# Kernel optimization log

Measured on AMD Instinct MI355X. Metric: run time of the kernel, lower is better.

The kernel has to match this reference:

```python
import jax, jax.numpy as jnp
import numpy as np

IN_CH, OUT_CH = 32, 32
MODES1, MODES2 = 16, 16
B, L, H, W = 8, 16, 64, 33


def setup_inputs() -> dict:
    key = jax.random.key(0)
    k = jax.random.split(key, 6)
    scale = 1.0 / (IN_CH * OUT_CH)
    wshape = (IN_CH, OUT_CH, MODES1, MODES2)
    return {
        "x_re": jax.random.normal(k[0], (B, L, IN_CH, H, W), dtype=jnp.float32),
        "x_im": jax.random.normal(k[1], (B, L, IN_CH, H, W), dtype=jnp.float32),
        "w1_re": scale * jax.random.normal(k[2], wshape, dtype=jnp.float32),
        "w1_im": scale * jax.random.normal(k[3], wshape, dtype=jnp.float32),
        "w2_re": scale * jax.random.normal(k[4], wshape, dtype=jnp.float32),
        "w2_im": scale * jax.random.normal(k[5], wshape, dtype=jnp.float32),
    }


def _mul2d(x, w):
    # x: [B, L, C_in, m1, m2] complex; w: [C_in, C_out, m1, m2] complex
    return jnp.einsum("blcij,coij->bloij", x, w)


def reference(x_re, x_im, w1_re, w1_im, w2_re, w2_im):
    x = jax.lax.complex(x_re, x_im)          # [B, L, C, H, W] complex64
    w1 = jax.lax.complex(w1_re, w1_im)       # [C_in, C_out, m1, m2]
    w2 = jax.lax.complex(w2_re, w2_im)
    Bx, Lx, Cx, Hx, Wx = x.shape
    m1 = min(Hx, MODES1)
    m2 = min(Wx, MODES2)

    out = jnp.zeros((Bx, Lx, OUT_CH, Hx, Wx), dtype=x.dtype)
    # low positive frequencies (top-left corner)
    out = out.at[:, :, :, :m1, :m2].set(
        _mul2d(x[:, :, :, :m1, :m2], w1[:, :, :m1, :m2]))
    # low negative frequencies along H (bottom-left corner)
    if Hx > 1 and (Hx > MODES1 or Wx > MODES2):
        out = out.at[:, :, :, -m1:, :m2].set(
            _mul2d(x[:, :, :, -m1:, :m2], w2[:, :, :m1, :m2]))
    # return complex result as trailing real/imag dim (float32)
    return jnp.stack([out.real, out.imag], axis=-1)
```

## Files before the change

### kernel.cpp

```cpp
#include <hip/hip_runtime.h>

#define IN_CH 32
#define OUT_CH 32
#define M1 16
#define M2 16
#define H_ 64
#define W_ 33
#define HW (H_*W_)
#define BLPB 4
#define WSTRIDE (OUT_CH*M1*M2)
#define CBATCH 8

__global__ __launch_bounds__(256) void spectral_fused(
    const float* __restrict__ x_re, const float* __restrict__ x_im,
    const float* __restrict__ w1_re, const float* __restrict__ w1_im,
    const float* __restrict__ w2_re, const float* __restrict__ w2_im,
    float* __restrict__ out)
{
    const int tid = threadIdx.x;

    if (blockIdx.x & 1) {
        const int fid = blockIdx.x >> 1;
        const int gtid = fid * 256 + tid;
        const int nthreads = 1024 * 256;

        float4* out4 = (float4*)out;
        const float4 z4 = make_float4(0.f, 0.f, 0.f, 0.f);
        const int totalA = 4096 * 528;
        for (int idx = gtid; idx < totalA; idx += nthreads) {
            int plane = idx / 528;
            int k = idx - plane * 528;
            out4[(long)plane * 1056 + 264 + k] = z4;
        }
        float2* out2 = (float2*)out;
        const float2 z2 = make_float2(0.f, 0.f);
        const int totalB = 4096 * 544;
        for (int idx = gtid; idx < totalB; idx += nthreads) {
            int plane = idx / 544;
            int r = idx - plane * 544;
            int hh = r / 17;
            int t = r - hh * 17;
            int h = hh < 16 ? hh : hh + 32;
            out2[(long)plane * 2112 + h * 33 + 16 + t] = z2;
        }
        return;
    }

    const int cid = blockIdx.x >> 1;
    const int ri = cid >> 5;
    const int chunk = cid & 31;
    const int region = ri >> 4;
    const int i = ri & 15;
    const int h = region ? (48 + i) : i;
    const int bl0 = chunk * BLPB;

    __shared__ float2 xs[BLPB][IN_CH][M2];

    for (int item = tid; item < BLPB * IN_CH * M2; item += 256) {
        int j = item & 15;
        int c = (item >> 4) & 31;
        int b = item >> 9;
        long src = (long)((bl0 + b) * IN_CH + c) * HW + (long)h * W_ + j;
        xs[b][c][j] = make_float2(x_re[src], x_im[src]);
    }
    __syncthreads();

    const int j  = tid & 15;
    const int o0 = tid >> 4;
    const float* __restrict__ wre = (region ? w2_re : w1_re) + (o0 * M1 + i) * M2 + j;
    const float* __restrict__ wim = (region ? w2_im : w1_im) + (o0 * M1 + i) * M2 + j;

    float2 acc0[BLPB], acc1[BLPB];
    #pragma unroll
    for (int b = 0; b < BLPB; ++b) {
        acc0[b] = make_float2(0.f, 0.f);
        acc1[b] = make_float2(0.f, 0.f);
    }

    #pragma unroll 1
    for (int cb = 0; cb < IN_CH; cb += CBATCH) {
        float wr0[CBATCH], wi0[CBATCH], wr1[CBATCH], wi1[CBATCH];
        #pragma unroll
        for (int u = 0; u < CBATCH; ++u) {
            int idx = (cb + u) * WSTRIDE;
            wr0[u] = wre[idx];        wi0[u] = wim[idx];
            wr1[u] = wre[idx + 4096]; wi1[u] = wim[idx + 4096];
        }
        #pragma unroll
        for (int u = 0; u < CBATCH; ++u) {
            #pragma unroll
            for (int b = 0; b < BLPB; ++b) {
                float2 xc = xs[b][cb + u][j];
                acc0[b].x = fmaf(xc.x, wr0[u], acc0[b].x); acc0[b].x = fmaf(-xc.y, wi0[u], acc0[b].x);
                acc0[b].y = fmaf(xc.x, wi0[u], acc0[b].y); acc0[b].y = fmaf( xc.y, wr0[u], acc0[b].y);
                acc1[b].x = fmaf(xc.x, wr1[u], acc1[b].x); acc1[b].x = fmaf(-xc.y, wi1[u], acc1[b].x);
                acc1[b].y = fmaf(xc.x, wi1[u], acc1[b].y); acc1[b].y = fmaf( xc.y, wr1[u], acc1[b].y);
            }
        }
    }

    float2* out2 = (float2*)out;
    #pragma unroll
    for (int b = 0; b < BLPB; ++b) {
        long plane = (long)(bl0 + b) * OUT_CH;
        long d0 = (plane + o0)      * HW + (long)h * W_ + j;
        long d1 = (plane + o0 + 16) * HW + (long)h * W_ + j;
        out2[d0] = acc0[b];
        out2[d1] = acc1[b];
    }
}

extern "C" void kernel_launch(void* const* d_in, const int* in_sizes, int n_in,
                              void* d_out, int out_size, void* d_ws, size_t ws_size,
                              hipStream_t stream) {
    const float* x_re  = (const float*)d_in[0];
    const float* x_im  = (const float*)d_in[1];
    const float* w1_re = (const float*)d_in[2];
    const float* w1_im = (const float*)d_in[3];
    const float* w2_re = (const float*)d_in[4];
    const float* w2_im = (const float*)d_in[5];
    float* out = (float*)d_out;

    spectral_fused<<<dim3(2048), dim3(256), 0, stream>>>(
        x_re, x_im, w1_re, w1_im, w2_re, w2_im, out);
}
```

Baseline: 37.14 us.

## Use bf16x3-split MFMA for the complex mode contraction with a prep kernel

Replaces the scalar FMA complex contraction with two kernels. The first gathers the mode slices of x and the weights, splits each fp32 value into hi and lo bf16 parts, and stores them in a workspace in MFMA fragment layout. The second runs 16x16x32 bf16 MFMAs, using three products per real term to approximate fp32 accuracy, and writes the combined real and imaginary outputs. The zero-fill of the output is split between the two kernels. In exchange it adds a second launch and a round trip through the workspace, and the bf16 split may lose a little precision compared with fp32.

```diff
diff --git a/kernel.cpp b/kernel.cpp
--- a/kernel.cpp
+++ b/kernel.cpp
@@ -1,112 +1,200 @@
 #include <hip/hip_runtime.h>
 
-#define IN_CH 32
-#define OUT_CH 32
-#define M1 16
-#define M2 16
-#define H_ 64
-#define W_ 33
-#define HW (H_*W_)
-#define BLPB 4
-#define WSTRIDE (OUT_CH*M1*M2)
-#define CBATCH 8
-
-__global__ __launch_bounds__(256) void spectral_fused(
+#define HW 2112L
+typedef float f32x4 __attribute__((ext_vector_type(4)));
+typedef short s16x8 __attribute__((ext_vector_type(8)));
+
+#define XT_PLANE 4194304L
+#define WT_PLANE 1048576L
+#define OFF_XHR 0L
+#define OFF_XLR (XT_PLANE)
+#define OFF_XHI (2*XT_PLANE)
+#define OFF_XLI (3*XT_PLANE)
+#define OFF_WHR (4*XT_PLANE)
+#define OFF_WLR (4*XT_PLANE + WT_PLANE)
+#define OFF_WHI (4*XT_PLANE + 2*WT_PLANE)
+#define OFF_WLI (4*XT_PLANE + 3*WT_PLANE)
+
+__device__ __forceinline__ ushort f2bf(float f) {
+    unsigned u = __float_as_uint(f);
+    u += 0x7FFF + ((u >> 16) & 1);
+    return (ushort)(u >> 16);
+}
+__device__ __forceinline__ void split_bf(float v, ushort& hi, ushort& lo) {
+    hi = f2bf(v);
+    float hf = __uint_as_float(((unsigned)hi) << 16);
+    lo = f2bf(v - hf);
+}
+
+__global__ __launch_bounds__(256) void spectral_prep(
     const float* __restrict__ x_re, const float* __restrict__ x_im,
     const float* __restrict__ w1_re, const float* __restrict__ w1_im,
     const float* __restrict__ w2_re, const float* __restrict__ w2_im,
-    float* __restrict__ out)
+    float* __restrict__ out, char* __restrict__ ws)
 {
     const int tid = threadIdx.x;
-
-    if (blockIdx.x & 1) {
-        const int fid = blockIdx.x >> 1;
-        const int gtid = fid * 256 + tid;
-        const int nthreads = 1024 * 256;
-
+    const int bid = blockIdx.x;
+    __shared__ float lds[32][16][17];
+
+    if (bid < 256) {
+        const int r = bid >> 7, i = (bid >> 3) & 15, mt = bid & 7;
+        const int h = r ? 48 + i : i;
+        const int j = tid >> 4, row = tid & 15;
+        const int modeLin = (r * 16 + i) * 16 + j;
+        #pragma unroll 1
+        for (int pass = 0; pass < 2; ++pass) {
+            const float* src = pass ? x_im : x_re;
+            if (pass) __syncthreads();
+            for (int it = 0; it < 32; ++it) {
+                int idx = it * 256 + tid;
+                int jj = idx & 15, rr = idx >> 4;
+                int c = rr >> 4, rw = rr & 15;
+                int bl = mt * 16 + rw;
+                lds[c][rw][jj] = src[(long)(bl * 32 + c) * HW + h * 33 + jj];
+            }
+            __syncthreads();
+            s16x8* ph = (s16x8*)(ws + (pass ? OFF_XHI : OFF_XHR));
+            s16x8* pl = (s16x8*)(ws + (pass ? OFF_XLI : OFF_XLR));
+            #pragma unroll
+            for (int kg = 0; kg < 4; ++kg) {
+                s16x8 vh, vl;
+                #pragma unroll
+                for (int e = 0; e < 8; ++e) {
+                    ushort a, b;
+                    split_bf(lds[kg * 8 + e][row][j], a, b);
+                    vh[e] = (short)a; vl[e] = (short)b;
+                }
+                long off = (long)(modeLin * 8 + mt) * 64 + kg * 16 + row;
+                ph[off] = vh;
+                pl[off] = vl;
+            }
+        }
+    } else if (bid < 320) {
+        const int widx = bid - 256;
+        const int r = widx >> 5, i = (widx >> 1) & 15, nt = widx & 1;
+        const float* wre = r ? w2_re : w1_re;
+        const float* wim = r ? w2_im : w1_im;
+        const int j = tid >> 4, col = tid & 15, o = nt * 16 + col;
+        const int modeLin = (r * 16 + i) * 16 + j;
+        s16x8* phr = (s16x8*)(ws + OFF_WHR);
+        s16x8* plr = (s16x8*)(ws + OFF_WLR);
+        s16x8* phi = (s16x8*)(ws + OFF_WHI);
+        s16x8* pli = (s16x8*)(ws + OFF_WLI);
+        #pragma unroll
+        for (int kg = 0; kg < 4; ++kg) {
+            s16x8 hr, lr, hi2, li2;
+            #pragma unroll
+            for (int e = 0; e < 8; ++e) {
+                int c = kg * 8 + e;
+                long src = ((long)(c * 32 + o) * 16 + i) * 16 + j;
+                ushort a, b;
+                split_bf(wre[src], a, b); hr[e] = (short)a; lr[e] = (short)b;
+                split_bf(wim[src], a, b); hi2[e] = (short)a; li2[e] = (short)b;
+            }
+            long off = (long)(modeLin * 2 + nt) * 64 + kg * 16 + col;
+            phr[off] = hr; plr[off] = lr; phi[off] = hi2; pli[off] = li2;
+        }
+    } else {
+        const int fid = bid - 320;
+        int gtid = fid * 256 + tid, n = 512 * 256;
         float4* out4 = (float4*)out;
-        const float4 z4 = make_float4(0.f, 0.f, 0.f, 0.f);
-        const int totalA = 4096 * 528;
-        for (int idx = gtid; idx < totalA; idx += nthreads) {
+        const float4 z = make_float4(0.f, 0.f, 0.f, 0.f);
+        for (int idx = gtid; idx < 4096 * 528; idx += n) {
             int plane = idx / 528;
             int k = idx - plane * 528;
-            out4[(long)plane * 1056 + 264 + k] = z4;
-        }
+            out4[(long)plane * 1056 + 264 + k] = z;
+        }
+    }
+}
+
+__global__ __launch_bounds__(256) void spectral_mfma(
+    float* __restrict__ out, const char* __restrict__ ws)
+{
+    const int tid = threadIdx.x, bid = blockIdx.x;
+
+    if (bid >= 512) {
+        const int fid = bid - 512;
+        int gtid = fid * 256 + tid, n = 512 * 256;
         float2* out2 = (float2*)out;
-        const float2 z2 = make_float2(0.f, 0.f);
-        const int totalB = 4096 * 544;
-        for (int idx = gtid; idx < totalB; idx += nthreads) {
+        const float2 z = make_float2(0.f, 0.f);
+        for (int idx = gtid; idx < 4096 * 544; idx += n) {
             int plane = idx / 544;
-            int r = idx - plane * 544;
-            int hh = r / 17;
-            int t = r - hh * 17;
+            int rr = idx - plane * 544;
+            int hh = rr / 17, t = rr - hh * 17;
             int h = hh < 16 ? hh : hh + 32;
-            out2[(long)plane * 2112 + h * 33 + 16 + t] = z2;
+            out2[(long)plane * 2112 + h * 33 + 16 + t] = z;
         }
         return;
     }
 
-    const int cid = blockIdx.x >> 1;
-    const int ri = cid >> 5;
-    const int chunk = cid & 31;
-    const int region = ri >> 4;
-    const int i = ri & 15;
-    const int h = region ? (48 + i) : i;
-    const int bl0 = chunk * BLPB;
-
-    __shared__ float2 xs[BLPB][IN_CH][M2];
-
-    for (int item = tid; item < BLPB * IN_CH * M2; item += 256) {
-        int j = item & 15;
-        int c = (item >> 4) & 31;
-        int b = item >> 9;
-        long src = (long)((bl0 + b) * IN_CH + c) * HW + (long)h * W_ + j;
-        xs[b][c][j] = make_float2(x_re[src], x_im[src]);
-    }
-    __syncthreads();
-
-    const int j  = tid & 15;
-    const int o0 = tid >> 4;
-    const float* __restrict__ wre = (region ? w2_re : w1_re) + (o0 * M1 + i) * M2 + j;
-    const float* __restrict__ wim = (region ? w2_im : w1_im) + (o0 * M1 + i) * M2 + j;
-
-    float2 acc0[BLPB], acc1[BLPB];
-    #pragma unroll
-    for (int b = 0; b < BLPB; ++b) {
-        acc0[b] = make_float2(0.f, 0.f);
-        acc1[b] = make_float2(0.f, 0.f);
-    }
-
-    #pragma unroll 1
-    for (int cb = 0; cb < IN_CH; cb += CBATCH) {
-        float wr0[CBATCH], wi0[CBATCH], wr1[CBATCH], wi1[CBATCH];
-        #pragma unroll
-        for (int u = 0; u < CBATCH; ++u) {
-            int idx = (cb + u) * WSTRIDE;
-            wr0[u] = wre[idx];        wi0[u] = wim[idx];
-            wr1[u] = wre[idx + 4096]; wi1[u] = wim[idx + 4096];
-        }
-        #pragma unroll
-        for (int u = 0; u < CBATCH; ++u) {
+    const int r = bid >> 8, i = (bid >> 4) & 15, j = bid & 15;
+    const int h = r ? 48 + i : i;
+    const int modeLin = (r * 16 + i) * 16 + j;
+    const int wave = tid >> 6, lane = tid & 63;
+
+    const s16x8* Axhr = (const s16x8*)(ws + OFF_XHR);
+    const s16x8* Axlr = (const s16x8*)(ws + OFF_XLR);
+    const s16x8* Axhi = (const s16x8*)(ws + OFF_XHI);
+    const s16x8* Axli = (const s16x8*)(ws + OFF_XLI);
+    const s16x8* Bwhr = (const s16x8*)(ws + OFF_WHR);
+    const s16x8* Bwlr = (const s16x8*)(ws + OFF_WLR);
+    const s16x8* Bwhi = (const s16x8*)(ws + OFF_WHI);
+    const s16x8* Bwli = (const s16x8*)(ws + OFF_WLI);
+
+    s16x8 Bhr[2], Blr[2], Bhi[2], Bli[2];
+    #pragma unroll
+    for (int nt = 0; nt < 2; ++nt) {
+        long boff = (long)(modeLin * 2 + nt) * 64 + lane;
+        Bhr[nt] = Bwhr[boff]; Blr[nt] = Bwlr[boff];
+        Bhi[nt] = Bwhi[boff]; Bli[nt] = Bwli[boff];
+    }
+
+    f32x4 accP[2][2], accN[2][2], accI[2][2];
+    #pragma unroll
+    for (int m = 0; m < 2; ++m)
+        #pragma unroll
+        for (int nt = 0; nt < 2; ++nt) {
+            accP[m][nt] = (f32x4)0.0f; accN[m][nt] = (f32x4)0.0f; accI[m][nt] = (f32x4)0.0f;
+        }
+
+    #pragma unroll
+    for (int m = 0; m < 2; ++m) {
+        const int mt = wave * 2 + m;
+        long aoff = (long)(modeLin * 8 + mt) * 64 + lane;
+        s16x8 Ahr = Axhr[aoff], Alr = Axlr[aoff];
+        s16x8 Ahi = Axhi[aoff], Ali = Axli[aoff];
+        #pragma unroll
+        for (int nt = 0; nt < 2; ++nt) {
+            accP[m][nt] = __builtin_amdgcn_mfma_f32_16x16x32_bf16(Ahr, Bhr[nt], accP[m][nt], 0, 0, 0);
+            accP[m][nt] = __builtin_amdgcn_mfma_f32_16x16x32_bf16(Ahr, Blr[nt], accP[m][nt], 0, 0, 0);
+            accP[m][nt] = __builtin_amdgcn_mfma_f32_16x16x32_bf16(Alr, Bhr[nt], accP[m][nt], 0, 0, 0);
+            accN[m][nt] = __builtin_amdgcn_mfma_f32_16x16x32_bf16(Ahi, Bhi[nt], accN[m][nt], 0, 0, 0);
+            accN[m][nt] = __builtin_amdgcn_mfma_f32_16x16x32_bf16(Ahi, Bli[nt], accN[m][nt], 0, 0, 0);
+            accN[m][nt] = __builtin_amdgcn_mfma_f32_16x16x32_bf16(Ali, Bhi[nt], accN[m][nt], 0, 0, 0);
+            accI[m][nt] = __builtin_amdgcn_mfma_f32_16x16x32_bf16(Ahr, Bhi[nt], accI[m][nt], 0, 0, 0);
+            accI[m][nt] = __builtin_amdgcn_mfma_f32_16x16x32_bf16(Ahr, Bli[nt], accI[m][nt], 0, 0, 0);
+            accI[m][nt] = __builtin_amdgcn_mfma_f32_16x16x32_bf16(Alr, Bhi[nt], accI[m][nt], 0, 0, 0);
+            accI[m][nt] = __builtin_amdgcn_mfma_f32_16x16x32_bf16(Ahi, Bhr[nt], accI[m][nt], 0, 0, 0);
+            accI[m][nt] = __builtin_amdgcn_mfma_f32_16x16x32_bf16(Ahi, Blr[nt], accI[m][nt], 0, 0, 0);
+            accI[m][nt] = __builtin_amdgcn_mfma_f32_16x16x32_bf16(Ali, Bhr[nt], accI[m][nt], 0, 0, 0);
+        }
+    }
+
+    float2* out2 = (float2*)out;
+    const int colo = lane & 15, rbase = (lane >> 4) * 4;
+    #pragma unroll
+    for (int m = 0; m < 2; ++m) {
+        const int mt = wave * 2 + m;
+        #pragma unroll
+        for (int nt = 0; nt < 2; ++nt) {
+            const int o = nt * 16 + colo;
             #pragma unroll
-            for (int b = 0; b < BLPB; ++b) {
-                float2 xc = xs[b][cb + u][j];
-                acc0[b].x = fmaf(xc.x, wr0[u], acc0[b].x); acc0[b].x = fmaf(-xc.y, wi0[u], acc0[b].x);
-                acc0[b].y = fmaf(xc.x, wi0[u], acc0[b].y); acc0[b].y = fmaf( xc.y, wr0[u], acc0[b].y);
-                acc1[b].x = fmaf(xc.x, wr1[u], acc1[b].x); acc1[b].x = fmaf(-xc.y, wi1[u], acc1[b].x);
-                acc1[b].y = fmaf(xc.x, wi1[u], acc1[b].y); acc1[b].y = fmaf( xc.y, wr1[u], acc1[b].y);
-            }
-        }
-    }
-
-    float2* out2 = (float2*)out;
-    #pragma unroll
-    for (int b = 0; b < BLPB; ++b) {
-        long plane = (long)(bl0 + b) * OUT_CH;
-        long d0 = (plane + o0)      * HW + (long)h * W_ + j;
-        long d1 = (plane + o0 + 16) * HW + (long)h * W_ + j;
-        out2[d0] = acc0[b];
-        out2[d1] = acc1[b];
+            for (int q = 0; q < 4; ++q) {
+                int bl = mt * 16 + rbase + q;
+                long dst = ((long)(bl * 32 + o) * 64 + h) * 33 + j;
+                out2[dst] = make_float2(accP[m][nt][q] - accN[m][nt][q], accI[m][nt][q]);
+            }
+        }
     }
 }
 
@@ -120,7 +208,9 @@
     const float* w2_re = (const float*)d_in[4];
     const float* w2_im = (const float*)d_in[5];
     float* out = (float*)d_out;
-
-    spectral_fused<<<dim3(2048), dim3(256), 0, stream>>>(
-        x_re, x_im, w1_re, w1_im, w2_re, w2_im, out);
-}
+    char* ws = (char*)d_ws;
+
+    spectral_prep<<<dim3(832), dim3(256), 0, stream>>>(
+        x_re, x_im, w1_re, w1_im, w2_re, w2_im, out, ws);
+    spectral_mfma<<<dim3(1024), dim3(256), 0, stream>>>(out, ws);
+}
```

Measured after the change: 57.78 us. +55.6%, slower.
